# Kernel tuning notes

Hardware: AMD Instinct MI355X
Metric: run time of the kernel (lower is better)

## Reference

```python
import jax, jax.numpy as jnp
import numpy as np

B, C, T, H, W = 2, 512, 8, 16, 16
NUM_HEADS = 8
HEAD_DIM = C // NUM_HEADS


def setup_inputs() -> dict:
    key = jax.random.key(0)
    ks = jax.random.split(key, 6)
    x = jax.random.normal(ks[0], (B, C, T, H, W), dtype=jnp.float32)
    # LayerNorm params
    ln_w = jnp.ones((C,), dtype=jnp.float32)
    ln_b = jnp.zeros((C,), dtype=jnp.float32)
    # 1x1x1 Conv3d == per-token linear; weight stored [out, in]
    w_qkv = jax.random.normal(ks[1], (3 * C, C), dtype=jnp.float32) * (1.0 / np.sqrt(C))
    b_qkv = jnp.zeros((3 * C,), dtype=jnp.float32)
    w_proj = jax.random.normal(ks[2], (C, C), dtype=jnp.float32) * (1.0 / np.sqrt(C))
    b_proj = jnp.zeros((C,), dtype=jnp.float32)
    return {"x": x, "ln_w": ln_w, "ln_b": ln_b, "w_qkv": w_qkv,
            "b_qkv": b_qkv, "w_proj": w_proj, "b_proj": b_proj}


def reference(x, ln_w, ln_b, w_qkv, b_qkv, w_proj, b_proj):
    Bx, Cx, Tx, Hx, Wx = x.shape
    N = Tx * Hx * Wx
    scale = HEAD_DIM ** -0.5

    # [B,C,T,H,W] -> [B,N,C]
    x_flat = jnp.transpose(x, (0, 2, 3, 4, 1)).reshape(Bx, N, Cx)

    # LayerNorm over channels
    mu = jnp.mean(x_flat, axis=-1, keepdims=True)
    var = jnp.var(x_flat, axis=-1, keepdims=True)
    x_flat = (x_flat - mu) * jax.lax.rsqrt(var + 1e-5) * ln_w + ln_b

    # QKV (1x1x1 conv == linear). Output channel layout: [3, heads, head_dim]
    qkv = jnp.einsum('bnc,oc->bno', x_flat, w_qkv) + b_qkv  # [B,N,3C]
    qkv = qkv.reshape(Bx, N, 3, NUM_HEADS, HEAD_DIM)
    qkv = jnp.transpose(qkv, (2, 0, 3, 1, 4))  # [3,B,heads,N,head_dim]
    q, k, v = qkv[0], qkv[1], qkv[2]

    attn = jnp.einsum('bhnd,bhmd->bhnm', q, k) * scale
    attn = jax.nn.softmax(attn, axis=-1)
    x_attn = jnp.einsum('bhnm,bhmd->bhnd', attn, v)  # [B,heads,N,head_dim]
    x_attn = jnp.transpose(x_attn, (0, 2, 1, 3)).reshape(Bx, N, Cx)

    # proj (1x1x1 conv == linear)
    x_attn = jnp.einsum('bnc,oc->bno', x_attn, w_proj) + b_proj

    # NOTE: residual is on the *normalized* x_flat (as in the original module)
    x_out = x_flat + x_attn
    x_out = x_out.reshape(Bx, Tx, Hx, Wx, Cx)
    return jnp.transpose(x_out, (0, 4, 1, 2, 3))  # [B,C,T,H,W]
```

## Files before the change

### kernel.cpp

```cpp
#include <hip/hip_runtime.h>
#include <hip/hip_bf16.h>

#define BB 2
#define CC 512
#define NN 2048
#define NHEADS 8
#define HDIM 64
#define NSPLIT 4
#define KVQ 512

typedef __attribute__((ext_vector_type(8))) __bf16 bf16x8;
typedef __attribute__((ext_vector_type(4))) __bf16 bf16x4;
typedef __attribute__((ext_vector_type(2))) __bf16 bf16x2;
typedef __attribute__((ext_vector_type(4))) float f32x4;

typedef const __attribute__((address_space(1))) unsigned int guint;
typedef __attribute__((address_space(3))) unsigned int suint;

#define QSCALE 0.18033688f
#define MX3(a, b, c) fmaxf(fmaxf(a, b), c)

__global__ __launch_bounds__(256) void ln_fused_kernel(
    const float* __restrict__ x, const float* __restrict__ lnw,
    const float* __restrict__ lnb, float* __restrict__ mu,
    float* __restrict__ rstd, __bf16* __restrict__ xln_t) {
  __shared__ float Xs[512][20];
  __shared__ float rs[16][17];
  __shared__ float rq[16][17];
  __shared__ float mloc[16];
  __shared__ float rloc[16];
  int bid = blockIdx.x;
  int n_tile = 2 * (((bid >> 4) << 3) + (bid & 7)) + ((bid >> 3) & 1);
  int n0 = n_tile * 16;
  int b = blockIdx.y;
  int tid = threadIdx.x;
#pragma unroll
  for (int l = 0; l < 8; ++l) {
    int e = tid + 256 * l;
    int row = e >> 2, quad = e & 3;
    float4 v = *(const float4*)&x[((size_t)b * CC + row) * NN + n0 + quad * 4];
    *(float4*)&Xs[row][quad * 4] = v;
  }
  __syncthreads();
  {
    int tk = tid & 15, part = tid >> 4;
    float s = 0.f, ss = 0.f;
    int c0 = part * 32;
#pragma unroll 8
    for (int j = 0; j < 32; ++j) {
      float v = Xs[c0 + j][tk];
      s += v;
      ss += v * v;
    }
    rs[part][tk] = s;
    rq[part][tk] = ss;
  }
  __syncthreads();
  if (tid < 16) {
    float S = 0.f, SS = 0.f;
#pragma unroll
    for (int p = 0; p < 16; ++p) {
      S += rs[p][tid];
      SS += rq[p][tid];
    }
    float m = S * (1.0f / CC);
    float var = SS * (1.0f / CC) - m * m;
    float rv = rsqrtf(var + 1e-5f);
    mloc[tid] = m;
    rloc[tid] = rv;
    int tok = b * NN + n0 + tid;
    mu[tok] = m;
    rstd[tok] = rv;
  }
  __syncthreads();
  {
    int tk = tid >> 4;
    int cseg = (tid & 15) * 32;
    float mun = mloc[tk], rsn = rloc[tk];
    __bf16 outv[32];
#pragma unroll
    for (int j = 0; j < 32; ++j) {
      int c = cseg + j;
      outv[j] = (__bf16)((Xs[c][tk] - mun) * rsn * lnw[c] + lnb[c]);
    }
    __bf16* dst = &xln_t[((size_t)b * NN + n0 + tk) * CC + cseg];
#pragma unroll
    for (int q = 0; q < 4; ++q) *(bf16x8*)&dst[q * 8] = *(bf16x8*)&outv[q * 8];
  }
}

__global__ __launch_bounds__(256) void qkv_mfma_kernel(
    const __bf16* __restrict__ xln_t, const float* __restrict__ w,
    const float* __restrict__ bias, __bf16* __restrict__ qt,
    __bf16* __restrict__ kt, __bf16* __restrict__ vbf) {
  __shared__ __align__(16) __bf16 As[2][64][68];
  __shared__ __align__(16) __bf16 Bs[2][128][68];
  int n0 = blockIdx.x * 128;
  bool swap = blockIdx.y < 16;
  int m0 = swap ? blockIdx.y * 64 : 1024 + ((int)blockIdx.y - 16) * 64;
  int b = blockIdx.z;
  int tid = threadIdx.x;
  int wid = tid >> 6, lane = tid & 63;
  int g = lane >> 4, c = lane & 15;
  int wr = wid >> 1, wc = wid & 1;
  const __bf16* xln = xln_t + (size_t)b * NN * CC;
  int arow = tid >> 4, ac4 = tid & 15;
  int brow = tid >> 3, bc8 = tid & 7;

  float4 wA[4];
  bf16x8 xB[4];
  auto LOADREGS = [&](int k0) {
#pragma unroll
    for (int l = 0; l < 4; ++l)
      wA[l] = *(const float4*)&w[(size_t)(m0 + arow + 16 * l) * CC + k0 + ac4 * 4];
#pragma unroll
    for (int l = 0; l < 4; ++l)
      xB[l] = *(const bf16x8*)&xln[(size_t)(n0 + brow + 32 * l) * CC + k0 + bc8 * 8];
  };
  auto STORELDS = [&](int buf) {
#pragma unroll
    for (int l = 0; l < 4; ++l) {
      bf16x4 pk = {(__bf16)wA[l].x, (__bf16)wA[l].y, (__bf16)wA[l].z,
                   (__bf16)wA[l].w};
      *(bf16x4*)&As[buf][arow + 16 * l][ac4 * 4] = pk;
    }
#pragma unroll
    for (int l = 0; l < 4; ++l)
      *(bf16x8*)&Bs[buf][brow + 32 * l][bc8 * 8] = xB[l];
  };

  LOADREGS(0);
  STORELDS(0);
  __syncthreads();
  f32x4 acc[2][4] = {};
  for (int ktile = 0; ktile < 8; ++ktile) {
    int cur = ktile & 1;
    if (ktile < 7) LOADREGS((ktile + 1) * 64);
#pragma unroll
    for (int hh = 0; hh < 2; ++hh) {
      bf16x8 af[2], bfr[4];
#pragma unroll
      for (int mi = 0; mi < 2; ++mi)
        af[mi] = *(const bf16x8*)&As[cur][wr * 32 + mi * 16 + c][hh * 32 + g * 8];
#pragma unroll
      for (int nj = 0; nj < 4; ++nj)
        bfr[nj] = *(const bf16x8*)&Bs[cur][wc * 64 + nj * 16 + c][hh * 32 + g * 8];
      if (swap) {
#pragma unroll
        for (int mi = 0; mi < 2; ++mi)
#pragma unroll
          for (int nj = 0; nj < 4; ++nj)
            acc[mi][nj] = __builtin_amdgcn_mfma_f32_16x16x32_bf16(
                bfr[nj], af[mi], acc[mi][nj], 0, 0, 0);
      } else {
#pragma unroll
        for (int mi = 0; mi < 2; ++mi)
#pragma unroll
          for (int nj = 0; nj < 4; ++nj)
            acc[mi][nj] = __builtin_amdgcn_mfma_f32_16x16x32_bf16(
                af[mi], bfr[nj], acc[mi][nj], 0, 0, 0);
      }
    }
    if (ktile < 7) STORELDS(cur ^ 1);
    __syncthreads();
  }
  if (swap) {
    int obase = m0 + wr * 32;
    int sec = obase >> 9;
    int osec = obase & 511;
    int head = osec >> 6;
    int dbase = osec & 63;
    __bf16* dst = (sec == 0 ? qt : kt) + (size_t)(b * NHEADS + head) * NN * HDIM;
    float scl = (sec == 0) ? QSCALE : 1.0f;
#pragma unroll
    for (int mi = 0; mi < 2; ++mi) {
      float bo = bias[obase + mi * 16 + c];
      int d = dbase + mi * 16 + c;
#pragma unroll
      for (int nj = 0; nj < 4; ++nj)
#pragma unroll
        for (int r = 0; r < 4; ++r) {
          int n = n0 + wc * 64 + nj * 16 + 4 * g + r;
          dst[(size_t)n * HDIM + d] = (__bf16)((acc[mi][nj][r] + bo) * scl);
        }
    }
  } else {
#pragma unroll
    for (int mi = 0; mi < 2; ++mi)
#pragma unroll
      for (int r = 0; r < 4; ++r) {
        int o = m0 + wr * 32 + mi * 16 + 4 * g + r;
        int ch = o - 1024;
        float bo = bias[o];
#pragma unroll
        for (int nj = 0; nj < 4; ++nj) {
          int n = n0 + wc * 64 + nj * 16 + c;
          vbf[((size_t)b * CC + ch) * NN + n] = (__bf16)(acc[mi][nj][r] + bo);
        }
      }
  }
}

__global__ __launch_bounds__(256, 3) void attn_mfma_kernel(
    const __bf16* __restrict__ qt, const __bf16* __restrict__ ktg,
    const __bf16* __restrict__ vbf, __bf16* __restrict__ opart,
    float* __restrict__ ml) {
  __shared__ __align__(16) __bf16 Kb[2][64][64];
  __shared__ __align__(16) __bf16 Vb[2][64][64];
  int tid = threadIdx.x;
  int wid = tid >> 6, lane = tid & 63;
  int g = lane >> 4, c = lane & 15;
  int n0 = blockIdx.x * 128;
  int h = blockIdx.y;
  int b = blockIdx.z >> 2, split = blockIdx.z & 3;
  int bh = b * NHEADS + h;
  const __bf16* qbase = qt + ((size_t)bh * NN + n0) * HDIM;
  const __bf16* kbase = ktg + ((size_t)bh * NN + split * KVQ) * HDIM;
  const __bf16* vbase = vbf + ((size_t)b * CC + h * HDIM) * NN + split * KVQ;

  int l7 = lane & 7, l3 = lane >> 3;
  int xr = (l7 ^ l3) * 8;
  auto STAGE = [&](int buf, int mt) {
#pragma unroll
    for (int j = 0; j < 2; ++j) {
      int r = wid * 16 + 8 * j + l3;
      int gr = (r & 0x20) | (((r >> 2) & 3) << 3) | (((r >> 4) & 1) << 2) | (r & 3);
      const __bf16* ksrc = kbase + (size_t)(mt + gr) * HDIM + xr;
      __builtin_amdgcn_global_load_lds((guint*)ksrc,
                                       (suint*)&Kb[buf][wid * 16 + 8 * j][0],
                                       16, 0, 0);
      const __bf16* vsrc = vbase + (size_t)r * NN + mt + xr;
      __builtin_amdgcn_global_load_lds((guint*)vsrc,
                                       (suint*)&Vb[buf][wid * 16 + 8 * j][0],
                                       16, 0, 0);
    }
  };

  STAGE(0, 0);
  bf16x8 aq[2][2];
#pragma unroll
  for (int qg = 0; qg < 2; ++qg) {
    const __bf16* qp = qbase + (size_t)(wid * 32 + qg * 16 + c) * HDIM;
    aq[qg][0] = *(const bf16x8*)(qp + g * 8);
    aq[qg][1] = *(const bf16x8*)(qp + 32 + g * 8);
  }
  f32x4 O[2][4] = {};
  f32x4 Ol[2] = {};
  float m_[2] = {-1e30f, -1e30f};
  int cxor = (c & 7);
  const bf16x8 vones = {(__bf16)1.f, (__bf16)1.f, (__bf16)1.f, (__bf16)1.f,
                        (__bf16)1.f, (__bf16)1.f, (__bf16)1.f, (__bf16)1.f};

  for (int t = 0; t < KVQ / 64; ++t) {
    int cur = t & 1;
    if (t + 1 < KVQ / 64) {
      STAGE(cur ^ 1, (t + 1) * 64);
      asm volatile("s_waitcnt vmcnt(4)" ::: "memory");
    } else {
      asm volatile("s_waitcnt vmcnt(0)" ::: "memory");
    }
    __builtin_amdgcn_sched_barrier(0);
    __builtin_amdgcn_s_barrier();
    f32x4 st[2][4];
    __builtin_amdgcn_s_setprio(1);
#pragma unroll
    for (int t4 = 0; t4 < 4; ++t4) {
      bf16x8 bk0 = *(const bf16x8*)&Kb[cur][t4 * 16 + c][(g ^ cxor) * 8];
      bf16x8 bk1 = *(const bf16x8*)&Kb[cur][t4 * 16 + c][((4 + g) ^ cxor) * 8];
#pragma unroll
      for (int qg = 0; qg < 2; ++qg) {
        f32x4 acc = {0.f, 0.f, 0.f, 0.f};
        acc = __builtin_amdgcn_mfma_f32_16x16x32_bf16(bk0, aq[qg][0], acc, 0, 0, 0);
        acc = __builtin_amdgcn_mfma_f32_16x16x32_bf16(bk1, aq[qg][1], acc, 0, 0, 0);
        st[qg][t4] = acc;
      }
    }
    __builtin_amdgcn_s_setprio(0);
    bf16x8 pa[2][2];
#pragma unroll
    for (int qg = 0; qg < 2; ++qg) {
      float g0 = MX3(st[qg][0][0], st[qg][0][1], st[qg][0][2]);
      float g1 = MX3(st[qg][0][3], st[qg][1][0], st[qg][1][1]);
      float g2 = MX3(st[qg][1][2], st[qg][1][3], st[qg][2][0]);
      float g3 = MX3(st[qg][2][1], st[qg][2][2], st[qg][2][3]);
      float g4 = MX3(st[qg][3][0], st[qg][3][1], st[qg][3][2]);
      float pm = fmaxf(MX3(g0, g1, g2), MX3(g3, g4, st[qg][3][3]));
      if (!__all(pm <= m_[qg] + 8.0f)) {
        float rm = fmaxf(pm, __shfl_xor(pm, 16));
        rm = fmaxf(rm, __shfl_xor(rm, 32));
        float mn = fmaxf(m_[qg], rm);
        float fs = exp2f(m_[qg] - mn);
        m_[qg] = mn;
#pragma unroll
        for (int dt = 0; dt < 4; ++dt)
#pragma unroll
          for (int r = 0; r < 4; ++r) O[qg][dt][r] *= fs;
#pragma unroll
        for (int r = 0; r < 4; ++r) Ol[qg][r] *= fs;
      }
#pragma unroll
      for (int t4 = 0; t4 < 4; ++t4) {
        float p0 = exp2f(st[qg][t4][0] - m_[qg]);
        float p1 = exp2f(st[qg][t4][1] - m_[qg]);
        float p2 = exp2f(st[qg][t4][2] - m_[qg]);
        float p3 = exp2f(st[qg][t4][3] - m_[qg]);
        bf16x8* pp = &pa[qg][t4 >> 1];
        int o4 = (t4 & 1) * 4;
        (*pp)[o4 + 0] = (__bf16)p0;
        (*pp)[o4 + 1] = (__bf16)p1;
        (*pp)[o4 + 2] = (__bf16)p2;
        (*pp)[o4 + 3] = (__bf16)p3;
      }
    }
    __builtin_amdgcn_s_setprio(1);
#pragma unroll
    for (int dt = 0; dt < 4; ++dt) {
      bf16x8 bv0 = *(const bf16x8*)&Vb[cur][dt * 16 + c][(g ^ cxor) * 8];
      bf16x8 bv1 = *(const bf16x8*)&Vb[cur][dt * 16 + c][((4 + g) ^ cxor) * 8];
#pragma unroll
      for (int qg = 0; qg < 2; ++qg) {
        O[qg][dt] = __builtin_amdgcn_mfma_f32_16x16x32_bf16(bv0, pa[qg][0],
                                                            O[qg][dt], 0, 0, 0);
        O[qg][dt] = __builtin_amdgcn_mfma_f32_16x16x32_bf16(bv1, pa[qg][1],
                                                            O[qg][dt], 0, 0, 0);
      }
    }
#pragma unroll
    for (int qg = 0; qg < 2; ++qg) {
      Ol[qg] = __builtin_amdgcn_mfma_f32_16x16x32_bf16(vones, pa[qg][0],
                                                       Ol[qg], 0, 0, 0);
      Ol[qg] = __builtin_amdgcn_mfma_f32_16x16x32_bf16(vones, pa[qg][1],
                                                       Ol[qg], 0, 0, 0);
    }
    __builtin_amdgcn_s_setprio(0);
    __builtin_amdgcn_s_barrier();
  }
#pragma unroll
  for (int qg = 0; qg < 2; ++qg) {
    size_t prow = ((size_t)(split * BB + b) * NHEADS + h) * NN +
                  (n0 + wid * 32 + qg * 16 + c);
#pragma unroll
    for (int dt = 0; dt < 4; ++dt) {
      bf16x4 pk = {(__bf16)O[qg][dt][0], (__bf16)O[qg][dt][1],
                   (__bf16)O[qg][dt][2], (__bf16)O[qg][dt][3]};
      *(bf16x4*)&opart[prow * HDIM + dt * 16 + 4 * g] = pk;
    }
    if (lane < 16) {
      float2 mlv = {m_[qg], Ol[qg][0]};
      *(float2*)&ml[prow * 2] = mlv;
    }
  }
}

__global__ __launch_bounds__(256) void attn_combine_kernel(
    const __bf16* __restrict__ opart, const float* __restrict__ ml,
    __bf16* __restrict__ xa_t) {
  int t = threadIdx.x;
  int row_local = t >> 4;
  int dq = (t & 15) * 4;
  int R = blockIdx.x * 16 + row_local;
  int n = R & (NN - 1);
  int bh = R >> 11;
  int b = bh >> 3, h = bh & 7;
  size_t ps[NSPLIT];
  float ms[NSPLIT], ls[NSPLIT];
  float m = -1e30f;
#pragma unroll
  for (int s = 0; s < NSPLIT; ++s) {
    ps[s] = ((size_t)(s * BB + b) * NHEADS + h) * NN + n;
    ms[s] = ml[ps[s] * 2];
    ls[s] = ml[ps[s] * 2 + 1];
    m = fmaxf(m, ms[s]);
  }
  float lsum = 0.f;
  float ws[NSPLIT];
#pragma unroll
  for (int s = 0; s < NSPLIT; ++s) {
    ws[s] = exp2f(ms[s] - m);
    lsum += ls[s] * ws[s];
  }
  float linv = 1.0f / lsum;
  float acc[4] = {0.f, 0.f, 0.f, 0.f};
#pragma unroll
  for (int s = 0; s < NSPLIT; ++s) {
    bf16x4 ov = *(const bf16x4*)&opart[ps[s] * HDIM + dq];
#pragma unroll
    for (int j = 0; j < 4; ++j) acc[j] += (float)ov[j] * ws[s];
  }
  bf16x4 pk = {(__bf16)(acc[0] * linv), (__bf16)(acc[1] * linv),
               (__bf16)(acc[2] * linv), (__bf16)(acc[3] * linv)};
  *(bf16x4*)&xa_t[((size_t)b * NN + n) * CC + h * HDIM + dq] = pk;
}

__global__ __launch_bounds__(256) void proj_mfma_kernel(
    const __bf16* __restrict__ xa_t, const float* __restrict__ w,
    const float* __restrict__ bias, const float* __restrict__ x,
    const float* __restrict__ mu, const float* __restrict__ rstd,
    const float* __restrict__ lnw, const float* __restrict__ lnb,
    float* __restrict__ out) {
  __shared__ __align__(16) __bf16 As[2][64][68];
  __shared__ __align__(16) __bf16 Bs[2][64][68];
  int n0 = blockIdx.x * 64;
  int m0 = blockIdx.y * 64;
  int b = blockIdx.z;
  int tid = threadIdx.x;
  int wid = tid >> 6, lane = tid & 63;
  int g = lane >> 4, c = lane & 15;
  int wr = wid >> 1, wc = wid & 1;
  const __bf16* xab = xa_t + (size_t)b * NN * CC;
  int arow = tid >> 4, ac4 = tid & 15;
  int brow = tid >> 3, bc8 = tid & 7;

  float4 wA[4];
  bf16x8 xB[2];
  auto LOADREGS = [&](int k0) {
#pragma unroll
    for (int l = 0; l < 4; ++l)
      wA[l] = *(const float4*)&w[(size_t)(m0 + arow + 16 * l) * CC + k0 + ac4 * 4];
#pragma unroll
    for (int l = 0; l < 2; ++l)
      xB[l] = *(const bf16x8*)&xab[(size_t)(n0 + brow + 32 * l) * CC + k0 + bc8 * 8];
  };
  auto STORELDS = [&](int buf) {
#pragma unroll
    for (int l = 0; l < 4; ++l) {
      bf16x4 pk = {(__bf16)wA[l].x, (__bf16)wA[l].y, (__bf16)wA[l].z,
                   (__bf16)wA[l].w};
      *(bf16x4*)&As[buf][arow + 16 * l][ac4 * 4] = pk;
    }
#pragma unroll
    for (int l = 0; l < 2; ++l)
      *(bf16x8*)&Bs[buf][brow + 32 * l][bc8 * 8] = xB[l];
  };

  LOADREGS(0);
  STORELDS(0);
  __syncthreads();
  f32x4 acc[2][2] = {};
  for (int ktile = 0; ktile < 8; ++ktile) {
    int cur = ktile & 1;
    if (ktile < 7) LOADREGS((ktile + 1) * 64);
#pragma unroll
    for (int hh = 0; hh < 2; ++hh) {
      bf16x8 af[2], bfr[2];
#pragma unroll
      for (int mi = 0; mi < 2; ++mi)
        af[mi] = *(const bf16x8*)&As[cur][wr * 32 + mi * 16 + c][hh * 32 + g * 8];
#pragma unroll
      for (int nj = 0; nj < 2; ++nj)
        bfr[nj] = *(const bf16x8*)&Bs[cur][wc * 32 + nj * 16 + c][hh * 32 + g * 8];
#pragma unroll
      for (int mi = 0; mi < 2; ++mi)
#pragma unroll
        for (int nj = 0; nj < 2; ++nj)
          acc[mi][nj] = __builtin_amdgcn_mfma_f32_16x16x32_bf16(
              af[mi], bfr[nj], acc[mi][nj], 0, 0, 0);
    }
    if (ktile < 7) STORELDS(cur ^ 1);
    __syncthreads();
  }
#pragma unroll
  for (int mi = 0; mi < 2; ++mi)
#pragma unroll
    for (int r = 0; r < 4; ++r) {
      int o = m0 + wr * 32 + mi * 16 + 4 * g + r;
      float bo = bias[o], gw = lnw[o], gb = lnb[o];
#pragma unroll
      for (int nj = 0; nj < 2; ++nj) {
        int n = n0 + wc * 32 + nj * 16 + c;
        int tok = b * NN + n;
        float xv = x[((size_t)b * CC + o) * NN + n];
        float xlnv = (xv - mu[tok]) * rstd[tok] * gw + gb;
        out[((size_t)b * CC + o) * NN + n] = acc[mi][nj][r] + bo + xlnv;
      }
    }
}

extern "C" void kernel_launch(void* const* d_in, const int* in_sizes, int n_in,
                              void* d_out, int out_size, void* d_ws, size_t ws_size,
                              hipStream_t stream) {
  const float* x = (const float*)d_in[0];
  const float* lnw = (const float*)d_in[1];
  const float* lnb = (const float*)d_in[2];
  const float* wqkv = (const float*)d_in[3];
  const float* bqkv = (const float*)d_in[4];
  const float* wproj = (const float*)d_in[5];
  const float* bproj = (const float*)d_in[6];
  float* out = (float*)d_out;
  (void)in_sizes; (void)n_in; (void)out_size; (void)ws_size;

  char* wsb = (char*)d_ws;
  float* mu = (float*)wsb;
  float* rstd = mu + 4096;
  const size_t HSZ = (size_t)BB * NHEADS * NN * HDIM;
  __bf16* qt = (__bf16*)(wsb + 32768);
  __bf16* kt = qt + HSZ;
  __bf16* vbf = kt + HSZ;
  __bf16* xa_t = vbf + HSZ;
  __bf16* xln_t = xa_t + HSZ;
  __bf16* opart = xln_t;
  float* ml = (float*)(wsb + 32768 + 4 * HSZ * sizeof(__bf16) +
                       (size_t)NSPLIT * HSZ * sizeof(__bf16));

  hipLaunchKernelGGL(ln_fused_kernel, dim3(128, 2), dim3(256), 0, stream,
                     x, lnw, lnb, mu, rstd, xln_t);
  hipLaunchKernelGGL(qkv_mfma_kernel, dim3(16, 24, 2), dim3(256), 0, stream,
                     xln_t, wqkv, bqkv, qt, kt, vbf);
  hipLaunchKernelGGL(attn_mfma_kernel, dim3(16, 8, BB * NSPLIT), dim3(256), 0,
                     stream, qt, kt, vbf, opart, ml);
  hipLaunchKernelGGL(attn_combine_kernel, dim3(2048), dim3(256), 0, stream,
                     opart, ml, xa_t);
  hipLaunchKernelGGL(proj_mfma_kernel, dim3(32, 8, 2), dim3(256), 0, stream,
                     xa_t, wproj, bproj, x, mu, rstd, lnw, lnb, out);
}
```

Baseline: 77.53 us.

## Pre-convert weights to bf16 and stage GEMM tiles with direct global-to-LDS loads

Adds a kernel that converts the QKV and projection weights to bf16 on every call. Both GEMM kernels now stage tiles with global_load_lds into XOR-swizzled unpadded LDS, using explicit vmcnt waits, raw barriers and setprio in place of register staging. This removes register round-trips and conversion from the inner loop. The attention KV split also drops from 4 to 2, which shrinks the combine work but also the grid parallelism. It costs one extra kernel launch and extra workspace for the bf16 weights.

```diff
diff --git a/kernel.cpp b/kernel.cpp
--- a/kernel.cpp
+++ b/kernel.cpp
@@ -6,12 +6,11 @@
 #define NN 2048
 #define NHEADS 8
 #define HDIM 64
-#define NSPLIT 4
-#define KVQ 512
+#define NSPLIT 2
+#define KVQ 1024
 
 typedef __attribute__((ext_vector_type(8))) __bf16 bf16x8;
 typedef __attribute__((ext_vector_type(4))) __bf16 bf16x4;
-typedef __attribute__((ext_vector_type(2))) __bf16 bf16x2;
 typedef __attribute__((ext_vector_type(4))) float f32x4;
 
 typedef const __attribute__((address_space(1))) unsigned int guint;
@@ -19,6 +18,23 @@
 
 #define QSCALE 0.18033688f
 #define MX3(a, b, c) fmaxf(fmaxf(a, b), c)
+
+__global__ __launch_bounds__(256) void cvt_w_kernel(
+    const float* __restrict__ wqkv, const float* __restrict__ wproj,
+    __bf16* __restrict__ wqkv_bf, __bf16* __restrict__ wproj_bf) {
+  int i = blockIdx.x * 256 + threadIdx.x;
+  const int NQ = 3 * CC * CC / 4;
+  if (i < NQ) {
+    float4 v = *(const float4*)&wqkv[(size_t)i * 4];
+    bf16x4 pk = {(__bf16)v.x, (__bf16)v.y, (__bf16)v.z, (__bf16)v.w};
+    *(bf16x4*)&wqkv_bf[(size_t)i * 4] = pk;
+  } else {
+    int j = i - NQ;
+    float4 v = *(const float4*)&wproj[(size_t)j * 4];
+    bf16x4 pk = {(__bf16)v.x, (__bf16)v.y, (__bf16)v.z, (__bf16)v.w};
+    *(bf16x4*)&wproj_bf[(size_t)j * 4] = pk;
+  }
+}
 
 __global__ __launch_bounds__(256) void ln_fused_kernel(
     const float* __restrict__ x, const float* __restrict__ lnw,
@@ -89,12 +105,12 @@
   }
 }
 
-__global__ __launch_bounds__(256) void qkv_mfma_kernel(
-    const __bf16* __restrict__ xln_t, const float* __restrict__ w,
+__global__ __launch_bounds__(256, 3) void qkv_mfma_kernel(
+    const __bf16* __restrict__ xln_t, const __bf16* __restrict__ wbf,
     const float* __restrict__ bias, __bf16* __restrict__ qt,
     __bf16* __restrict__ kt, __bf16* __restrict__ vbf) {
-  __shared__ __align__(16) __bf16 As[2][64][68];
-  __shared__ __align__(16) __bf16 Bs[2][128][68];
+  __shared__ __align__(16) __bf16 As[2][64][64];
+  __shared__ __align__(16) __bf16 Bs[2][128][64];
   int n0 = blockIdx.x * 128;
   bool swap = blockIdx.y < 16;
   int m0 = swap ? blockIdx.y * 64 : 1024 + ((int)blockIdx.y - 16) * 64;
@@ -104,47 +120,48 @@
   int g = lane >> 4, c = lane & 15;
   int wr = wid >> 1, wc = wid & 1;
   const __bf16* xln = xln_t + (size_t)b * NN * CC;
-  int arow = tid >> 4, ac4 = tid & 15;
-  int brow = tid >> 3, bc8 = tid & 7;
-
-  float4 wA[4];
-  bf16x8 xB[4];
-  auto LOADREGS = [&](int k0) {
-#pragma unroll
-    for (int l = 0; l < 4; ++l)
-      wA[l] = *(const float4*)&w[(size_t)(m0 + arow + 16 * l) * CC + k0 + ac4 * 4];
-#pragma unroll
-    for (int l = 0; l < 4; ++l)
-      xB[l] = *(const bf16x8*)&xln[(size_t)(n0 + brow + 32 * l) * CC + k0 + bc8 * 8];
+  int l7 = lane & 7, l3 = lane >> 3;
+  int xr = (l7 ^ l3) * 8;
+  auto STAGE = [&](int buf, int k0) {
+#pragma unroll
+    for (int j = 0; j < 2; ++j) {
+      int r = wid * 16 + 8 * j + l3;
+      __builtin_amdgcn_global_load_lds(
+          (guint*)(wbf + (size_t)(m0 + r) * CC + k0 + xr),
+          (suint*)&As[buf][wid * 16 + 8 * j][0], 16, 0, 0);
+    }
+#pragma unroll
+    for (int j = 0; j < 4; ++j) {
+      int r = wid * 32 + 8 * j + l3;
+      __builtin_amdgcn_global_load_lds(
+          (guint*)(xln + (size_t)(n0 + r) * CC + k0 + xr),
+          (suint*)&Bs[buf][wid * 32 + 8 * j][0], 16, 0, 0);
+    }
   };
-  auto STORELDS = [&](int buf) {
-#pragma unroll
-    for (int l = 0; l < 4; ++l) {
-      bf16x4 pk = {(__bf16)wA[l].x, (__bf16)wA[l].y, (__bf16)wA[l].z,
-                   (__bf16)wA[l].w};
-      *(bf16x4*)&As[buf][arow + 16 * l][ac4 * 4] = pk;
-    }
-#pragma unroll
-    for (int l = 0; l < 4; ++l)
-      *(bf16x8*)&Bs[buf][brow + 32 * l][bc8 * 8] = xB[l];
-  };
-
-  LOADREGS(0);
-  STORELDS(0);
-  __syncthreads();
+  STAGE(0, 0);
   f32x4 acc[2][4] = {};
-  for (int ktile = 0; ktile < 8; ++ktile) {
-    int cur = ktile & 1;
-    if (ktile < 7) LOADREGS((ktile + 1) * 64);
+  int cxor = c & 7;
+  for (int ks = 0; ks < 8; ++ks) {
+    int cur = ks & 1;
+    if (ks < 7) {
+      STAGE(cur ^ 1, (ks + 1) * 64);
+      asm volatile("s_waitcnt vmcnt(6)" ::: "memory");
+    } else {
+      asm volatile("s_waitcnt vmcnt(0)" ::: "memory");
+    }
+    __builtin_amdgcn_sched_barrier(0);
+    __builtin_amdgcn_s_barrier();
+    __builtin_amdgcn_s_setprio(1);
 #pragma unroll
     for (int hh = 0; hh < 2; ++hh) {
+      int ch = ((hh * 4 + g) ^ cxor) * 8;
       bf16x8 af[2], bfr[4];
 #pragma unroll
       for (int mi = 0; mi < 2; ++mi)
-        af[mi] = *(const bf16x8*)&As[cur][wr * 32 + mi * 16 + c][hh * 32 + g * 8];
+        af[mi] = *(const bf16x8*)&As[cur][wr * 32 + mi * 16 + c][ch];
 #pragma unroll
       for (int nj = 0; nj < 4; ++nj)
-        bfr[nj] = *(const bf16x8*)&Bs[cur][wc * 64 + nj * 16 + c][hh * 32 + g * 8];
+        bfr[nj] = *(const bf16x8*)&Bs[cur][wc * 64 + nj * 16 + c][ch];
       if (swap) {
 #pragma unroll
         for (int mi = 0; mi < 2; ++mi)
@@ -161,8 +178,8 @@
                 af[mi], bfr[nj], acc[mi][nj], 0, 0, 0);
       }
     }
-    if (ktile < 7) STORELDS(cur ^ 1);
-    __syncthreads();
+    __builtin_amdgcn_s_setprio(0);
+    __builtin_amdgcn_s_barrier();
   }
   if (swap) {
     int obase = m0 + wr * 32;
@@ -212,7 +229,7 @@
   int g = lane >> 4, c = lane & 15;
   int n0 = blockIdx.x * 128;
   int h = blockIdx.y;
-  int b = blockIdx.z >> 2, split = blockIdx.z & 3;
+  int b = blockIdx.z >> 1, split = blockIdx.z & 1;
   int bh = b * NHEADS + h;
   const __bf16* qbase = qt + ((size_t)bh * NN + n0) * HDIM;
   const __bf16* kbase = ktg + ((size_t)bh * NN + split * KVQ) * HDIM;
@@ -392,14 +409,14 @@
   *(bf16x4*)&xa_t[((size_t)b * NN + n) * CC + h * HDIM + dq] = pk;
 }
 
-__global__ __launch_bounds__(256) void proj_mfma_kernel(
-    const __bf16* __restrict__ xa_t, const float* __restrict__ w,
+__global__ __launch_bounds__(256, 4) void proj_mfma_kernel(
+    const __bf16* __restrict__ xa_t, const __bf16* __restrict__ wbf,
     const float* __restrict__ bias, const float* __restrict__ x,
     const float* __restrict__ mu, const float* __restrict__ rstd,
     const float* __restrict__ lnw, const float* __restrict__ lnb,
     float* __restrict__ out) {
-  __shared__ __align__(16) __bf16 As[2][64][68];
-  __shared__ __align__(16) __bf16 Bs[2][64][68];
+  __shared__ __align__(16) __bf16 As[2][64][64];
+  __shared__ __align__(16) __bf16 Bs[2][64][64];
   int n0 = blockIdx.x * 64;
   int m0 = blockIdx.y * 64;
   int b = blockIdx.z;
@@ -408,47 +425,44 @@
   int g = lane >> 4, c = lane & 15;
   int wr = wid >> 1, wc = wid & 1;
   const __bf16* xab = xa_t + (size_t)b * NN * CC;
-  int arow = tid >> 4, ac4 = tid & 15;
-  int brow = tid >> 3, bc8 = tid & 7;
-
-  float4 wA[4];
-  bf16x8 xB[2];
-  auto LOADREGS = [&](int k0) {
-#pragma unroll
-    for (int l = 0; l < 4; ++l)
-      wA[l] = *(const float4*)&w[(size_t)(m0 + arow + 16 * l) * CC + k0 + ac4 * 4];
-#pragma unroll
-    for (int l = 0; l < 2; ++l)
-      xB[l] = *(const bf16x8*)&xab[(size_t)(n0 + brow + 32 * l) * CC + k0 + bc8 * 8];
+  int l7 = lane & 7, l3 = lane >> 3;
+  int xr = (l7 ^ l3) * 8;
+  auto STAGE = [&](int buf, int k0) {
+#pragma unroll
+    for (int j = 0; j < 2; ++j) {
+      int r = wid * 16 + 8 * j + l3;
+      __builtin_amdgcn_global_load_lds(
+          (guint*)(wbf + (size_t)(m0 + r) * CC + k0 + xr),
+          (suint*)&As[buf][wid * 16 + 8 * j][0], 16, 0, 0);
+      __builtin_amdgcn_global_load_lds(
+          (guint*)(xab + (size_t)(n0 + r) * CC + k0 + xr),
+          (suint*)&Bs[buf][wid * 16 + 8 * j][0], 16, 0, 0);
+    }
   };
-  auto STORELDS = [&](int buf) {
-#pragma unroll
-    for (int l = 0; l < 4; ++l) {
-      bf16x4 pk = {(__bf16)wA[l].x, (__bf16)wA[l].y, (__bf16)wA[l].z,
-                   (__bf16)wA[l].w};
-      *(bf16x4*)&As[buf][arow + 16 * l][ac4 * 4] = pk;
-    }
-#pragma unroll
-    for (int l = 0; l < 2; ++l)
-      *(bf16x8*)&Bs[buf][brow + 32 * l][bc8 * 8] = xB[l];
-  };
-
-  LOADREGS(0);
-  STORELDS(0);
-  __syncthreads();
+  STAGE(0, 0);
   f32x4 acc[2][2] = {};
-  for (int ktile = 0; ktile < 8; ++ktile) {
-    int cur = ktile & 1;
-    if (ktile < 7) LOADREGS((ktile + 1) * 64);
+  int cxor = c & 7;
+  for (int ks = 0; ks < 8; ++ks) {
+    int cur = ks & 1;
+    if (ks < 7) {
+      STAGE(cur ^ 1, (ks + 1) * 64);
+      asm volatile("s_waitcnt vmcnt(4)" ::: "memory");
+    } else {
+      asm volatile("s_waitcnt vmcnt(0)" ::: "memory");
+    }
+    __builtin_amdgcn_sched_barrier(0);
+    __builtin_amdgcn_s_barrier();
+    __builtin_amdgcn_s_setprio(1);
 #pragma unroll
     for (int hh = 0; hh < 2; ++hh) {
+      int ch = ((hh * 4 + g) ^ cxor) * 8;
       bf16x8 af[2], bfr[2];
 #pragma unroll
       for (int mi = 0; mi < 2; ++mi)
-        af[mi] = *(const bf16x8*)&As[cur][wr * 32 + mi * 16 + c][hh * 32 + g * 8];
+        af[mi] = *(const bf16x8*)&As[cur][wr * 32 + mi * 16 + c][ch];
 #pragma unroll
       for (int nj = 0; nj < 2; ++nj)
-        bfr[nj] = *(const bf16x8*)&Bs[cur][wc * 32 + nj * 16 + c][hh * 32 + g * 8];
+        bfr[nj] = *(const bf16x8*)&Bs[cur][wc * 32 + nj * 16 + c][ch];
 #pragma unroll
       for (int mi = 0; mi < 2; ++mi)
 #pragma unroll
@@ -456,8 +470,8 @@
           acc[mi][nj] = __builtin_amdgcn_mfma_f32_16x16x32_bf16(
               af[mi], bfr[nj], acc[mi][nj], 0, 0, 0);
     }
-    if (ktile < 7) STORELDS(cur ^ 1);
-    __syncthreads();
+    __builtin_amdgcn_s_setprio(0);
+    __builtin_amdgcn_s_barrier();
   }
 #pragma unroll
   for (int mi = 0; mi < 2; ++mi)
@@ -498,18 +512,21 @@
   __bf16* vbf = kt + HSZ;
   __bf16* xa_t = vbf + HSZ;
   __bf16* xln_t = xa_t + HSZ;
-  __bf16* opart = xln_t;
-  float* ml = (float*)(wsb + 32768 + 4 * HSZ * sizeof(__bf16) +
-                       (size_t)NSPLIT * HSZ * sizeof(__bf16));
-
+  __bf16* opart = xln_t + HSZ;
+  float* ml = (float*)(opart + (size_t)NSPLIT * HSZ);
+  __bf16* wqkv_bf = (__bf16*)((char*)ml + 524288);
+  __bf16* wproj_bf = wqkv_bf + (size_t)3 * CC * CC;
+
+  hipLaunchKernelGGL(cvt_w_kernel, dim3(1024), dim3(256), 0, stream,
+                     wqkv, wproj, wqkv_bf, wproj_bf);
   hipLaunchKernelGGL(ln_fused_kernel, dim3(128, 2), dim3(256), 0, stream,
                      x, lnw, lnb, mu, rstd, xln_t);
   hipLaunchKernelGGL(qkv_mfma_kernel, dim3(16, 24, 2), dim3(256), 0, stream,
-                     xln_t, wqkv, bqkv, qt, kt, vbf);
+                     xln_t, wqkv_bf, bqkv, qt, kt, vbf);
   hipLaunchKernelGGL(attn_mfma_kernel, dim3(16, 8, BB * NSPLIT), dim3(256), 0,
                      stream, qt, kt, vbf, opart, ml);
   hipLaunchKernelGGL(attn_combine_kernel, dim3(2048), dim3(256), 0, stream,
                      opart, ml, xa_t);
   hipLaunchKernelGGL(proj_mfma_kernel, dim3(32, 8, 2), dim3(256), 0, stream,
-                     xa_t, wproj, bproj, x, mu, rstd, lnw, lnb, out);
-}
+                     xa_t, wproj_bf, bproj, x, mu, rstd, lnw, lnb, out);
+}
```

New measurement: 76.14 us. About the same (-1.8%).
